# Performance work log

Measured on AMD Instinct MI355X. Metric: run time of the kernel, lower is better.

Reference implementation:

```python
import jax, jax.numpy as jnp
import numpy as np

T, S, B, D, H, FFN = 1024, 1024, 4, 1024, 16, 4096
HD = D // H
EPS = 1e-5


def xavier(key, shape, gain=1.0):
    fan_out, fan_in = shape
    a = gain * np.sqrt(6.0 / (fan_in + fan_out))
    return jax.random.uniform(key, shape, jnp.float32, -a, a)


def layer_norm(x, g, b):
    mu = jnp.mean(x, axis=-1, keepdims=True)
    var = jnp.mean(jnp.square(x - mu), axis=-1, keepdims=True)
    return (x - mu) / jnp.sqrt(var + EPS) * g + b


def mha(q, k, v, Wq, bq, Wk, bk, Wv, bv, Wo, bo, key_padding_mask=None, attn_mask=None):
    # q: [t,b,d]; k,v: [s,b,d]; key_padding_mask: [b,s] bool (True = pad)
    t, b, d = q.shape
    s = v.shape[0]
    if key_padding_mask is not None:
        # original zeroes the KEY tensor before projection
        k = k * (~key_padding_mask).T[:, :, None]
    Q = (q @ Wq.T + bq).reshape(t, b, H, HD)
    K = (k @ Wk.T + bk).reshape(s, b, H, HD)
    V = (v @ Wv.T + bv).reshape(s, b, H, HD)
    scores = jnp.einsum('tbhk,sbhk->bhts', Q, K) / jnp.sqrt(jnp.float32(HD))
    if attn_mask is not None:
        scores = scores + attn_mask  # additive [t,s] broadcast over b,h
    p = jax.nn.softmax(scores, axis=-1)
    ctx = jnp.einsum('bhts,sbhk->tbhk', p, V)  # [t,b,h,hd]
    out = ctx.reshape(t, b, d)
    attn_w = jnp.swapaxes(ctx, 0, 2)  # [h,b,t,hd] as in original
    return out @ Wo.T + bo, attn_w


def setup_inputs() -> dict:
    key = jax.random.key(0)
    ks = jax.random.split(key, 16)
    inv2 = 1.0 / np.sqrt(2.0)
    d = {
        'state': jax.random.normal(ks[0], (T, B, D), jnp.float32),
        'encoder_out': jax.random.normal(ks[1], (S, B, D), jnp.float32),
        'self_attn_mask': jnp.triu(jnp.full((T, T), -1e9, jnp.float32), 1),
        'self_attn_padding_mask': jnp.zeros((B, T), bool),
        'encoder_padding_mask': jnp.broadcast_to(jnp.arange(S)[None, :] >= (S - S // 10), (B, S)),
        # self-attention projections
        'sa_Wq': xavier(ks[2], (D, D), inv2), 'sa_bq': jnp.zeros((D,), jnp.float32),
        'sa_Wk': xavier(ks[3], (D, D), inv2), 'sa_bk': jnp.zeros((D,), jnp.float32),
        'sa_Wv': xavier(ks[4], (D, D), inv2), 'sa_bv': jnp.zeros((D,), jnp.float32),
        'sa_Wo': xavier(ks[5], (D, D)), 'sa_bo': jnp.zeros((D,), jnp.float32),
        # encoder-decoder attention projections
        'ea_Wq': xavier(ks[6], (D, D), inv2), 'ea_bq': jnp.zeros((D,), jnp.float32),
        'ea_Wk': xavier(ks[7], (D, D), inv2), 'ea_bk': jnp.zeros((D,), jnp.float32),
        'ea_Wv': xavier(ks[8], (D, D), inv2), 'ea_bv': jnp.zeros((D,), jnp.float32),
        'ea_Wo': xavier(ks[9], (D, D)), 'ea_bo': jnp.zeros((D,), jnp.float32),
        # layernorms
        'ln1_g': jnp.ones((D,), jnp.float32), 'ln1_b': jnp.zeros((D,), jnp.float32),
        'ln2_g': jnp.ones((D,), jnp.float32), 'ln2_b': jnp.zeros((D,), jnp.float32),
        'ln3_g': jnp.ones((D,), jnp.float32), 'ln3_b': jnp.zeros((D,), jnp.float32),
        # FFN
        'fc1_W': xavier(ks[10], (FFN, D)), 'fc1_b': jnp.zeros((FFN,), jnp.float32),
        'fc2_W': xavier(ks[11], (D, FFN)), 'fc2_b': jnp.zeros((D,), jnp.float32),
    }
    return d


def reference(state, encoder_out, self_attn_mask, self_attn_padding_mask, encoder_padding_mask,
              sa_Wq, sa_bq, sa_Wk, sa_bk, sa_Wv, sa_bv, sa_Wo, sa_bo,
              ea_Wq, ea_bq, ea_Wk, ea_bk, ea_Wv, ea_bv, ea_Wo, ea_bo,
              ln1_g, ln1_b, ln2_g, ln2_b, ln3_g, ln3_b,
              fc1_W, fc1_b, fc2_W, fc2_b):
    x = state
    # self-attention block (dropout is identity in eval)
    res = x
    a, _ = mha(x, x, x, sa_Wq, sa_bq, sa_Wk, sa_bk, sa_Wv, sa_bv, sa_Wo, sa_bo,
               key_padding_mask=self_attn_padding_mask, attn_mask=self_attn_mask)
    x = layer_norm(a + res, ln1_g, ln1_b)
    # encoder-decoder attention block
    res = x
    a, attn = mha(x, encoder_out, encoder_out, ea_Wq, ea_bq, ea_Wk, ea_bk, ea_Wv, ea_bv, ea_Wo, ea_bo,
                  key_padding_mask=encoder_padding_mask, attn_mask=None)
    x = layer_norm(a + res, ln2_g, ln2_b)
    # FFN block
    res = x
    h = jax.nn.relu(x @ fc1_W.T + fc1_b)
    x = layer_norm(h @ fc2_W.T + fc2_b + res, ln3_g, ln3_b)
    return (x, attn)
```

## Files before the change

### kernel.cpp

```cpp
#include <hip/hip_runtime.h>
#include <hip/hip_bf16.h>


typedef __attribute__((ext_vector_type(8))) short bf16x8;
typedef __attribute__((ext_vector_type(4))) float f32x4;
typedef __attribute__((ext_vector_type(8))) unsigned short us8;
typedef __attribute__((ext_vector_type(4))) unsigned short us4;

#define AS1 __attribute__((address_space(1)))
#define AS3 __attribute__((address_space(3)))

#define T_LEN 1024
#define S_LEN 1024
#define B_DIM 4
#define D_MOD 1024
#define H_NUM 16
#define FFN_D 4096
#define NTOK  4096

__device__ __forceinline__ float b2f(unsigned short u) {
    return __uint_as_float(((unsigned int)u) << 16);
}
__device__ __forceinline__ unsigned short f2b(float f) {
    unsigned int x = __float_as_uint(f);
    x += 0x7fffu + ((x >> 16) & 1u);
    return (unsigned short)(x >> 16);
}

struct CvtArgs {
    const float* s[12];
    unsigned short* d[12];
};

__global__ __launch_bounds__(256) void cvt_all_kernel(CvtArgs a)
{
    const int cnt[12] = {2048, 2048, 512, 512, 512, 512, 512, 512, 512, 512, 2048, 2048};
    int bid = blockIdx.x;
    int seg = 0;
    while (bid >= cnt[seg]) { bid -= cnt[seg]; ++seg; }
    const size_t off = (size_t)bid * 2048 + threadIdx.x * 8;
    const float* src = a.s[seg] + off;
    unsigned short* dst = a.d[seg] + off;
    const f32x4 v0 = *(const f32x4*)src;
    const f32x4 v1 = *(const f32x4*)(src + 4);
    us8 o;
#pragma unroll
    for (int j = 0; j < 4; ++j) { o[j] = f2b(v0[j]); o[4 + j] = f2b(v1[j]); }
    *(us8*)dst = o;
}

template <int BN>
__global__ __launch_bounds__(512, 1) void gemm8ph_kernel(
    const unsigned short* __restrict__ A,
    const unsigned short* __restrict__ W,
    const float* __restrict__ b0, const float* __restrict__ b1,
    const float* __restrict__ b2, const float* __restrict__ b3,
    const int* __restrict__ rowmask, unsigned int maskbits,
    unsigned short* __restrict__ p0, unsigned short* __restrict__ p1,
    unsigned short* __restrict__ p2, unsigned short* __restrict__ p3,
    int ostride,
    const float* __restrict__ resid, float* __restrict__ outf,
    float* __restrict__ partf,
    int M, int N, int K, int relu, int ksplit)
{
    constexpr int NR  = BN / 64;
    constexpr int BLH = (BN * 64) / 8192;
    constexpr int BBUF = BN * 128;

    __shared__ __align__(16) char ldsb[65536 + 2 * BBUF];

    const int tid  = threadIdx.x;
    const int lane = tid & 63;
    const int wid  = tid >> 6;
    const int wr   = wid >> 2;
    const int wc   = wid & 3;
    const int row0 = blockIdx.x * 256;
    const int col0 = blockIdx.y * BN;
    const int rsel = lane & 15;
    const int kg2  = (lane >> 4) * 16;
    const int kz   = blockIdx.z;
    const int Keff = K / ksplit;
    const int koff = kz * Keff;
    const int NT   = Keff >> 6;

    f32x4 acc[8][NR];
#pragma unroll
    for (int m = 0; m < 8; ++m)
#pragma unroll
        for (int n = 0; n < NR; ++n)
            acc[m][n] = (f32x4){0.f, 0.f, 0.f, 0.f};

    auto stageA = [&](int buf, int half, int t) {
        const int k0 = koff + (t << 6);
#pragma unroll
        for (int i = 0; i < 2; ++i) {
            const unsigned int beta = (unsigned int)(half * 16384 + i * 8192 + tid * 16);
            const unsigned int lam  = beta ^ (((beta >> 7) & 7u) << 4);
            const char* src = (const char*)A +
                ((size_t)(row0 + (int)(lam >> 7)) * K + k0) * 2 + (lam & 127u);
            __builtin_amdgcn_global_load_lds((const AS1 void*)src,
                (AS3 void*)(ldsb + buf * 32768 + beta), 16, 0, 0);
        }
    };
    auto stageB = [&](int buf, int half, int t) {
        const int k0 = koff + (t << 6);
#pragma unroll
        for (int i = 0; i < BLH; ++i) {
            const unsigned int beta = (unsigned int)(half * (BN * 64) + i * 8192 + tid * 16);
            const unsigned int lam  = beta ^ (((beta >> 7) & 7u) << 4);
            const char* src = (const char*)W +
                ((size_t)(col0 + (int)(lam >> 7)) * K + k0) * 2 + (lam & 127u);
            __builtin_amdgcn_global_load_lds((const AS1 void*)src,
                (AS3 void*)(ldsb + 65536 + buf * BBUF + beta), 16, 0, 0);
        }
    };
    auto readA = [&](int buf, int m, int k) -> bf16x8 {
        const int r = wr * 128 + m * 16 + rsel;
        const unsigned int l  = (unsigned int)(r * 128 + k * 64 + kg2);
        const unsigned int ph = l ^ (((unsigned int)(r & 7)) << 4);
        return *(const bf16x8*)(ldsb + buf * 32768 + ph);
    };
    auto readB = [&](int buf, int n, int k) -> bf16x8 {
        const int r = wc * (BN / 4) + n * 16 + rsel;
        const unsigned int l  = (unsigned int)(r * 128 + k * 64 + kg2);
        const unsigned int ph = l ^ (((unsigned int)(r & 7)) << 4);
        return *(const bf16x8*)(ldsb + 65536 + buf * BBUF + ph);
    };

    stageA(0, 0, 0); stageA(0, 1, 0); stageB(0, 0, 0); stageB(0, 1, 0);
    stageA(1, 0, 1); stageA(1, 1, 1);
    asm volatile("s_waitcnt vmcnt(4)" ::: "memory");
    __builtin_amdgcn_s_barrier();

    bf16x8 Afr[8][2], Bfr[NR][2];

    for (int t = 0; t < NT; ++t) {
        const int cur = t & 1;
#pragma unroll
        for (int m = 0; m < 4; ++m) { Afr[m][0] = readA(cur, m, 0); Afr[m][1] = readA(cur, m, 1); }
#pragma unroll
        for (int n = 0; n < NR; ++n) Bfr[n][0] = readB(cur, n, 0);
        if (t + 1 < NT) stageB(cur ^ 1, 0, t + 1);
        __builtin_amdgcn_s_barrier();
        asm volatile("s_waitcnt lgkmcnt(0)" ::: "memory");
        __builtin_amdgcn_sched_barrier(0);
        __builtin_amdgcn_s_setprio(1);
#pragma unroll
        for (int m = 0; m < 4; ++m)
#pragma unroll
            for (int n = 0; n < NR; ++n)
                acc[m][n] = __builtin_amdgcn_mfma_f32_16x16x32_bf16(Afr[m][0], Bfr[n][0], acc[m][n], 0, 0, 0);
        __builtin_amdgcn_s_setprio(0);
        __builtin_amdgcn_s_barrier();
#pragma unroll
        for (int m = 4; m < 8; ++m) { Afr[m][0] = readA(cur, m, 0); Afr[m][1] = readA(cur, m, 1); }
#pragma unroll
        for (int n = 0; n < NR; ++n) Bfr[n][1] = readB(cur, n, 1);
        if (t + 1 < NT) stageB(cur ^ 1, 1, t + 1);
        __builtin_amdgcn_s_barrier();
        asm volatile("s_waitcnt lgkmcnt(0)" ::: "memory");
        __builtin_amdgcn_sched_barrier(0);
        __builtin_amdgcn_s_setprio(1);
#pragma unroll
        for (int m = 4; m < 8; ++m)
#pragma unroll
            for (int n = 0; n < NR; ++n)
                acc[m][n] = __builtin_amdgcn_mfma_f32_16x16x32_bf16(Afr[m][0], Bfr[n][0], acc[m][n], 0, 0, 0);
        __builtin_amdgcn_s_setprio(0);
        __builtin_amdgcn_s_barrier();
        if (t + 2 < NT) stageA(cur, 0, t + 2);
        __builtin_amdgcn_s_barrier();
        __builtin_amdgcn_s_setprio(1);
#pragma unroll
        for (int m = 0; m < 4; ++m)
#pragma unroll
            for (int n = 0; n < NR; ++n)
                acc[m][n] = __builtin_amdgcn_mfma_f32_16x16x32_bf16(Afr[m][1], Bfr[n][1], acc[m][n], 0, 0, 0);
        __builtin_amdgcn_s_setprio(0);
        __builtin_amdgcn_s_barrier();
        if (t + 2 < NT) stageA(cur, 1, t + 2);
        __builtin_amdgcn_s_barrier();
        __builtin_amdgcn_s_setprio(1);
#pragma unroll
        for (int m = 4; m < 8; ++m)
#pragma unroll
            for (int n = 0; n < NR; ++n)
                acc[m][n] = __builtin_amdgcn_mfma_f32_16x16x32_bf16(Afr[m][1], Bfr[n][1], acc[m][n], 0, 0, 0);
        __builtin_amdgcn_s_setprio(0);
        if (t + 2 < NT) { asm volatile("s_waitcnt vmcnt(4)" ::: "memory"); }
        else            { asm volatile("s_waitcnt vmcnt(0)" ::: "memory"); }
        __builtin_amdgcn_s_barrier();
    }

    const int seq  = M >> 2;
    const int c    = col0 >> 10;
    unsigned short* op = c == 0 ? p0 : c == 1 ? p1 : c == 2 ? p2 : p3;
    const float*    bp = c == 0 ? b0 : c == 1 ? b1 : c == 2 ? b2 : b3;
    const bool um = rowmask && ((maskbits >> c) & 1u);
    const int rbas = (lane >> 4) * 4;
    if (partf && kz > 0) {
#pragma unroll
        for (int m = 0; m < 8; ++m)
#pragma unroll
            for (int n = 0; n < NR; ++n)
#pragma unroll
                for (int j = 0; j < 4; ++j) {
                    const int gr = row0 + wr * 128 + m * 16 + rbas + j;
                    const int gc = col0 + wc * (BN / 4) + n * 16 + rsel;
                    partf[(size_t)gr * N + gc] = acc[m][n][j];
                }
    } else {
#pragma unroll
        for (int m = 0; m < 8; ++m)
#pragma unroll
            for (int n = 0; n < NR; ++n)
#pragma unroll
                for (int j = 0; j < 4; ++j) {
                    const int gr = row0 + wr * 128 + m * 16 + rbas + j;
                    const int gc = col0 + wc * (BN / 4) + n * 16 + rsel;
                    float v = acc[m][n][j];
                    if (um && rowmask[(gr & 3) * seq + (gr >> 2)] != 0) v = 0.f;
                    v += bp[gc & 1023];
                    if (relu) v = fmaxf(v, 0.f);
                    if (resid) v += resid[(size_t)gr * N + gc];
                    if (outf) outf[(size_t)gr * N + gc] = v;
                    else      op[(size_t)gr * ostride + (gc & 1023)] = f2b(v);
                }
    }
}

__global__ __launch_bounds__(256) void vtrans_kernel(
    const unsigned short* __restrict__ Vb, unsigned short* __restrict__ Vt)
{
    __shared__ unsigned short tile[64 * 72];
    const int tid = threadIdx.x;
    const int t0  = blockIdx.x * 64;
    const int bh  = blockIdx.y;
    const int h   = bh & (H_NUM - 1);
    const int b   = bh >> 4;

    const int r   = tid >> 2;
    const int c16 = (tid & 3) * 16;
    const unsigned short* src = Vb + ((size_t)(t0 + r) * B_DIM + b) * D_MOD + h * 64 + c16;
    *(us8*)&tile[r * 72 + c16]     = *(const us8*)src;
    *(us8*)&tile[r * 72 + c16 + 8] = *(const us8*)(src + 8);
    __syncthreads();

    const int dr  = tid >> 2;
    const int tch = (tid & 3) * 16;
    us8 o0, o1;
#pragma unroll
    for (int j = 0; j < 8; ++j) {
        o0[j] = tile[(tch + j) * 72 + dr];
        o1[j] = tile[(tch + 8 + j) * 72 + dr];
    }
    unsigned short* dst = Vt + (size_t)(bh * 64 + dr) * S_LEN + t0 + tch;
    *(us8*)dst       = o0;
    *(us8*)(dst + 8) = o1;
}

__global__ __launch_bounds__(256) void flash_mfma_kernel(
    const unsigned short* __restrict__ Qb,
    const unsigned short* __restrict__ Kb,
    const unsigned short* __restrict__ Vt,
    unsigned short* __restrict__ outc,
    float* __restrict__ outp,
    int causal)
{
    __shared__ __align__(16) unsigned short Ks[32 * 64];
    __shared__ __align__(16) unsigned short Vts[64 * 32];
    __shared__ __align__(16) unsigned short Ps[4 * 16 * 40];

    const int tid  = threadIdx.x;
    const int lane = tid & 63;
    const int wv   = tid >> 6;
    const int g    = lane >> 4;
    const int n    = lane & 15;
    const int t0   = blockIdx.x * 64;
    const int bh   = blockIdx.y;
    const int h    = bh & (H_NUM - 1);
    const int b    = bh >> 4;
    const int woff = wv * 16;

    bf16x8 qa[2];
    {
        const unsigned short* qptr =
            Qb + ((size_t)(t0 + woff + n) * B_DIM + b) * D_MOD + h * 64 + g * 8;
        qa[0] = *(const bf16x8*)qptr;
        qa[1] = *(const bf16x8*)(qptr + 32);
    }

    f32x4 ctx[4];
#pragma unroll
    for (int nt = 0; nt < 4; ++nt) ctx[nt] = (f32x4){0.f, 0.f, 0.f, 0.f};
    float m_run[4], l_run[4];
#pragma unroll
    for (int j = 0; j < 4; ++j) { m_run[j] = -INFINITY; l_run[j] = 0.f; }

    unsigned short* pw = &Ps[wv * 640];
    const int smax = causal ? (t0 + 64) : S_LEN;

    for (int s0 = 0; s0 < smax; s0 += 32) {
        {
            const unsigned int beta = tid * 16;
            const unsigned int lamK = beta ^ (((beta >> 7) & 7u) << 4);
            const unsigned int krow = lamK >> 7, kcolb = lamK & 127u;
            const char* srcK = (const char*)Kb +
                ((size_t)((s0 + krow) * B_DIM + b) * D_MOD + h * 64) * 2 + kcolb;
            __builtin_amdgcn_global_load_lds((const AS1 void*)srcK,
                (AS3 void*)((char*)Ks + beta), 16, 0, 0);
            const unsigned int lamV = beta ^ (((beta >> 6) & 3u) << 4);
            const unsigned int drow = lamV >> 6, scolb = lamV & 63u;
            const char* srcV = (const char*)Vt +
                ((size_t)(bh * 64 + drow) * S_LEN + s0) * 2 + scolb;
            __builtin_amdgcn_global_load_lds((const AS1 void*)srcV,
                (AS3 void*)((char*)Vts + beta), 16, 0, 0);
        }
        __syncthreads();

        f32x4 sacc[2];
        sacc[0] = (f32x4){0.f, 0.f, 0.f, 0.f};
        sacc[1] = (f32x4){0.f, 0.f, 0.f, 0.f};
#pragma unroll
        for (int u = 0; u < 2; ++u) {
#pragma unroll
            for (int kc = 0; kc < 2; ++kc) {
                const unsigned int l = (unsigned int)(u * 16 + n) * 128 + kc * 64 + g * 16;
                const unsigned int ph = l ^ ((unsigned int)(n & 7) << 4);
                const bf16x8 kb = *(const bf16x8*)((const char*)Ks + ph);
                sacc[u] = __builtin_amdgcn_mfma_f32_16x16x32_bf16(qa[kc], kb, sacc[u], 0, 0, 0);
            }
        }

        float e0[4], e1[4], scj[4];
#pragma unroll
        for (int j = 0; j < 4; ++j) {
            float p0 = sacc[0][j] * 0.125f;
            float p1 = sacc[1][j] * 0.125f;
            if (causal) {
                const int tq = t0 + woff + g * 4 + j;
                if (s0 + n > tq)      p0 += -1e9f;
                if (s0 + 16 + n > tq) p1 += -1e9f;
            }
            float mx = fmaxf(p0, p1);
            mx = fmaxf(mx, __shfl_xor(mx, 1));
            mx = fmaxf(mx, __shfl_xor(mx, 2));
            mx = fmaxf(mx, __shfl_xor(mx, 4));
            mx = fmaxf(mx, __shfl_xor(mx, 8));
            const float m_new = fmaxf(m_run[j], mx);
            const float sc = __expf(m_run[j] - m_new);
            m_run[j] = m_new;
            e0[j] = __expf(p0 - m_new);
            e1[j] = __expf(p1 - m_new);
            float ls = e0[j] + e1[j];
            ls += __shfl_xor(ls, 1);
            ls += __shfl_xor(ls, 2);
            ls += __shfl_xor(ls, 4);
            ls += __shfl_xor(ls, 8);
            l_run[j] = l_run[j] * sc + ls;
            scj[j] = sc;
        }
#pragma unroll
        for (int nt = 0; nt < 4; ++nt)
#pragma unroll
            for (int j = 0; j < 4; ++j) ctx[nt][j] *= scj[j];

#pragma unroll
        for (int j = 0; j < 4; ++j) {
            pw[(g * 4 + j) * 40 + n]      = f2b(e0[j]);
            pw[(g * 4 + j) * 40 + 16 + n] = f2b(e1[j]);
        }
        const bf16x8 pa = *(const bf16x8*)&pw[n * 40 + g * 8];

#pragma unroll
        for (int nt = 0; nt < 4; ++nt) {
            const unsigned int l = (unsigned int)(nt * 16 + n) * 64 + g * 16;
            const unsigned int ph = l ^ ((unsigned int)(n & 3) << 4);
            const bf16x8 vb = *(const bf16x8*)((const char*)Vts + ph);
            ctx[nt] = __builtin_amdgcn_mfma_f32_16x16x32_bf16(pa, vb, ctx[nt], 0, 0, 0);
        }
        __syncthreads();
    }

    float inv[4];
#pragma unroll
    for (int j = 0; j < 4; ++j) inv[j] = 1.f / l_run[j];
#pragma unroll
    for (int nt = 0; nt < 4; ++nt) {
#pragma unroll
        for (int j = 0; j < 4; ++j) {
            const int t = t0 + woff + g * 4 + j;
            const int d = nt * 16 + n;
            const float v = ctx[nt][j] * inv[j];
            outc[((size_t)t * B_DIM + b) * D_MOD + h * 64 + d] = f2b(v);
            if (outp)
                outp[((size_t)(h * B_DIM + b) * T_LEN + t) * 64 + d] = v;
        }
    }
}

__global__ __launch_bounds__(256) void layernorm_kernel(
    const float* __restrict__ y,
    const float* __restrict__ part,
    const float* __restrict__ g,
    const float* __restrict__ be,
    float* __restrict__ out_f,
    unsigned short* __restrict__ out_bf)
{
    __shared__ float red[8];
    const int row = blockIdx.x;
    const int tid = threadIdx.x;
    f32x4 v = *(const f32x4*)&y[(size_t)row * D_MOD + tid * 4];
    if (part) {
        const f32x4 pv = *(const f32x4*)&part[(size_t)row * D_MOD + tid * 4];
#pragma unroll
        for (int j = 0; j < 4; ++j) v[j] += pv[j];
    }
    float s = v[0] + v[1] + v[2] + v[3];
#pragma unroll
    for (int o = 32; o > 0; o >>= 1) s += __shfl_xor(s, o);
    if ((tid & 63) == 0) red[tid >> 6] = s;
    __syncthreads();
    const float mu = (red[0] + red[1] + red[2] + red[3]) * (1.f / D_MOD);
    const float d0 = v[0] - mu, d1 = v[1] - mu, d2 = v[2] - mu, d3 = v[3] - mu;
    float s2 = d0 * d0 + d1 * d1 + d2 * d2 + d3 * d3;
#pragma unroll
    for (int o = 32; o > 0; o >>= 1) s2 += __shfl_xor(s2, o);
    if ((tid & 63) == 0) red[4 + (tid >> 6)] = s2;
    __syncthreads();
    const float var  = (red[4] + red[5] + red[6] + red[7]) * (1.f / D_MOD);
    const float rstd = rsqrtf(var + 1e-5f);
    const float dd[4] = {d0, d1, d2, d3};
    f32x4 of;
    us4 ob;
#pragma unroll
    for (int j = 0; j < 4; ++j) {
        const int col = tid * 4 + j;
        const float r = dd[j] * rstd * g[col] + be[col];
        of[j] = r;
        ob[j] = f2b(r);
    }
    const size_t oi = (size_t)row * D_MOD + tid * 4;
    if (out_f)  *(f32x4*)&out_f[oi] = of;
    if (out_bf) *(us4*)&out_bf[oi]  = ob;
}

extern "C" void kernel_launch(void* const* d_in, const int* in_sizes, int n_in,
                              void* d_out, int out_size, void* d_ws, size_t ws_size,
                              hipStream_t stream) {
    (void)in_sizes; (void)n_in; (void)out_size; (void)ws_size;

    const float* x0    = (const float*)d_in[0];
    const float* enc   = (const float*)d_in[1];
    const int* sa_pad  = (const int*)d_in[3];
    const int* ea_pad  = (const int*)d_in[4];
    const float* sa_Wq = (const float*)d_in[5];
    const float* sa_bq = (const float*)d_in[6];
    const float* sa_Wk = (const float*)d_in[7];
    const float* sa_bk = (const float*)d_in[8];
    const float* sa_Wv = (const float*)d_in[9];
    const float* sa_bv = (const float*)d_in[10];
    const float* sa_Wo = (const float*)d_in[11];
    const float* sa_bo = (const float*)d_in[12];
    const float* ea_Wq = (const float*)d_in[13];
    const float* ea_bq = (const float*)d_in[14];
    const float* ea_Wk = (const float*)d_in[15];
    const float* ea_bk = (const float*)d_in[16];
    const float* ea_Wv = (const float*)d_in[17];
    const float* ea_bv = (const float*)d_in[18];
    const float* ea_Wo = (const float*)d_in[19];
    const float* ea_bo = (const float*)d_in[20];
    const float* ln1_g = (const float*)d_in[21];
    const float* ln1_b = (const float*)d_in[22];
    const float* ln2_g = (const float*)d_in[23];
    const float* ln2_b = (const float*)d_in[24];
    const float* ln3_g = (const float*)d_in[25];
    const float* ln3_b = (const float*)d_in[26];
    const float* fc1_W = (const float*)d_in[27];
    const float* fc1_b = (const float*)d_in[28];
    const float* fc2_W = (const float*)d_in[29];
    const float* fc2_b = (const float*)d_in[30];

    const size_t DD = (size_t)D_MOD * D_MOD;
    const size_t FD = (size_t)FFN_D * D_MOD;
    const size_t SL = (size_t)NTOK * D_MOD;

    unsigned short* ws_us = (unsigned short*)d_ws;
    unsigned short* wb[10];
    for (int i = 0; i < 8; ++i) wb[i] = ws_us + i * DD;
    wb[8] = ws_us + 8 * DD;
    wb[9] = ws_us + 8 * DD + FD;
    unsigned short* abf = ws_us + 8 * DD + 2 * FD;
    unsigned short* ebf = abf + SL;
    unsigned short* Cb  = ebf + SL;
    unsigned short* Qb  = Cb + SL;
    unsigned short* Kb  = Qb + SL;
    unsigned short* Vb  = Kb + SL;
    unsigned short* Vt  = Vb + SL;
    unsigned short* Hbf = Qb;
    float* fbase = (float*)(Vt + SL);
    float* Yf  = fbase;
    float* X1f = fbase + SL;
    float* Pq  = (float*)Qb;
    float* Pa  = (float*)abf;

    float* outx = (float*)d_out;
    float* outa = outx + SL;

    const dim3 blk(256);
    const dim3 blk512(512);
    const dim3 g_attn(T_LEN / 64, B_DIM * H_NUM);
    unsigned short* nbf = nullptr;
    float* nff = nullptr;
    const float* nf = nullptr;
    const int* ni = nullptr;

    {
        CvtArgs ca;
        const float* srcs[12]  = {x0, enc, sa_Wq, sa_Wk, sa_Wv, sa_Wo,
                                  ea_Wq, ea_Wk, ea_Wv, ea_Wo, fc1_W, fc2_W};
        unsigned short* dsts[12] = {abf, ebf, wb[0], wb[1], wb[2], wb[3],
                                    wb[4], wb[5], wb[6], wb[7], wb[8], wb[9]};
        for (int i = 0; i < 12; ++i) { ca.s[i] = srcs[i]; ca.d[i] = dsts[i]; }
        cvt_all_kernel<<<dim3(12288), blk, 0, stream>>>(ca);
    }

    gemm8ph_kernel<256><<<dim3(16, 12, 1), blk512, 0, stream>>>(
        abf, wb[0], sa_bq, sa_bk, sa_bv, sa_bv, sa_pad, 0x2u,
        Qb, Kb, Vb, Vb, D_MOD, nf, nff, nff, NTOK, 3072, D_MOD, 0, 1);
    vtrans_kernel<<<g_attn, blk, 0, stream>>>(Vb, Vt);
    flash_mfma_kernel<<<g_attn, blk, 0, stream>>>(Qb, Kb, Vt, Cb, nff, 1);
    gemm8ph_kernel<128><<<dim3(16, 8, 2), blk512, 0, stream>>>(
        Cb, wb[3], sa_bo, sa_bo, sa_bo, sa_bo, ni, 0u,
        nbf, nbf, nbf, nbf, D_MOD, x0, Yf, Pq, NTOK, D_MOD, D_MOD, 0, 2);
    layernorm_kernel<<<dim3(NTOK), blk, 0, stream>>>(Yf, Pq, ln1_g, ln1_b, X1f, abf);

    gemm8ph_kernel<128><<<dim3(16, 8, 1), blk512, 0, stream>>>(
        abf, wb[4], ea_bq, ea_bq, ea_bq, ea_bq, ni, 0u,
        Qb, Qb, Qb, Qb, D_MOD, nf, nff, nff, NTOK, D_MOD, D_MOD, 0, 1);
    gemm8ph_kernel<128><<<dim3(16, 16, 1), blk512, 0, stream>>>(
        ebf, wb[5], ea_bk, ea_bv, ea_bv, ea_bv, ea_pad, 0x1u,
        Kb, Vb, Vb, Vb, D_MOD, nf, nff, nff, NTOK, 2048, D_MOD, 0, 1);
    vtrans_kernel<<<g_attn, blk, 0, stream>>>(Vb, Vt);
    flash_mfma_kernel<<<g_attn, blk, 0, stream>>>(Qb, Kb, Vt, Cb, outa, 0);
    gemm8ph_kernel<128><<<dim3(16, 8, 2), blk512, 0, stream>>>(
        Cb, wb[7], ea_bo, ea_bo, ea_bo, ea_bo, ni, 0u,
        nbf, nbf, nbf, nbf, D_MOD, X1f, Yf, Pq, NTOK, D_MOD, D_MOD, 0, 2);
    layernorm_kernel<<<dim3(NTOK), blk, 0, stream>>>(Yf, Pq, ln2_g, ln2_b, X1f, ebf);

    gemm8ph_kernel<256><<<dim3(16, 16, 1), blk512, 0, stream>>>(
        ebf, wb[8], fc1_b, fc1_b + 1024, fc1_b + 2048, fc1_b + 3072, ni, 0u,
        Hbf, Hbf + 1024, Hbf + 2048, Hbf + 3072, FFN_D, nf, nff, nff,
        NTOK, FFN_D, D_MOD, 1, 1);
    gemm8ph_kernel<128><<<dim3(16, 8, 2), blk512, 0, stream>>>(
        Hbf, wb[9], fc2_b, fc2_b, fc2_b, fc2_b, ni, 0u,
        nbf, nbf, nbf, nbf, D_MOD, X1f, Yf, Pa, NTOK, D_MOD, FFN_D, 0, 2);
    layernorm_kernel<<<dim3(NTOK), blk, 0, stream>>>(Yf, Pa, ln3_g, ln3_b, outx, nbf);
}
```

Before: 703.3 us.

## Double-buffer K/V tiles and widen flash attention key tile to 64

```diff
diff --git a/kernel.cpp b/kernel.cpp
--- a/kernel.cpp
+++ b/kernel.cpp
@@ -259,7 +259,7 @@
     *(us8*)(dst + 8) = o1;
 }
 
-__global__ __launch_bounds__(256) void flash_mfma_kernel(
+__global__ __launch_bounds__(256, 3) void flash_mfma_kernel(
     const unsigned short* __restrict__ Qb,
     const unsigned short* __restrict__ Kb,
     const unsigned short* __restrict__ Vt,
@@ -267,9 +267,9 @@
     float* __restrict__ outp,
     int causal)
 {
-    __shared__ __align__(16) unsigned short Ks[32 * 64];
-    __shared__ __align__(16) unsigned short Vts[64 * 32];
-    __shared__ __align__(16) unsigned short Ps[4 * 16 * 40];
+    __shared__ __align__(16) unsigned short Ks[2][64 * 64];
+    __shared__ __align__(16) unsigned short Vts[2][64 * 64];
+    __shared__ __align__(16) unsigned short Ps[4][16 * 72];
 
     const int tid  = threadIdx.x;
     const int lane = tid & 63;
@@ -297,89 +297,106 @@
 #pragma unroll
     for (int j = 0; j < 4; ++j) { m_run[j] = -INFINITY; l_run[j] = 0.f; }
 
-    unsigned short* pw = &Ps[wv * 640];
+    unsigned short* pw = &Ps[wv][0];
     const int smax = causal ? (t0 + 64) : S_LEN;
-
-    for (int s0 = 0; s0 < smax; s0 += 32) {
-        {
-            const unsigned int beta = tid * 16;
-            const unsigned int lamK = beta ^ (((beta >> 7) & 7u) << 4);
-            const unsigned int krow = lamK >> 7, kcolb = lamK & 127u;
+    const int NTt  = smax >> 6;
+
+    auto stage = [&](int buf, int s0) {
+#pragma unroll
+        for (int i = 0; i < 2; ++i) {
+            const unsigned int beta = (unsigned int)(i * 4096 + tid * 16);
+            const unsigned int lam  = beta ^ (((beta >> 7) & 7u) << 4);
+            const int row = (int)(lam >> 7);
+            const unsigned int colb = lam & 127u;
             const char* srcK = (const char*)Kb +
-                ((size_t)((s0 + krow) * B_DIM + b) * D_MOD + h * 64) * 2 + kcolb;
+                ((size_t)((s0 + row) * B_DIM + b) * D_MOD + h * 64) * 2 + colb;
             __builtin_amdgcn_global_load_lds((const AS1 void*)srcK,
-                (AS3 void*)((char*)Ks + beta), 16, 0, 0);
-            const unsigned int lamV = beta ^ (((beta >> 6) & 3u) << 4);
-            const unsigned int drow = lamV >> 6, scolb = lamV & 63u;
+                (AS3 void*)((char*)&Ks[buf][0] + beta), 16, 0, 0);
             const char* srcV = (const char*)Vt +
-                ((size_t)(bh * 64 + drow) * S_LEN + s0) * 2 + scolb;
+                ((size_t)(bh * 64 + row) * S_LEN + s0) * 2 + colb;
             __builtin_amdgcn_global_load_lds((const AS1 void*)srcV,
-                (AS3 void*)((char*)Vts + beta), 16, 0, 0);
-        }
-        __syncthreads();
-
-        f32x4 sacc[2];
-        sacc[0] = (f32x4){0.f, 0.f, 0.f, 0.f};
-        sacc[1] = (f32x4){0.f, 0.f, 0.f, 0.f};
-#pragma unroll
-        for (int u = 0; u < 2; ++u) {
+                (AS3 void*)((char*)&Vts[buf][0] + beta), 16, 0, 0);
+        }
+    };
+
+    stage(0, 0);
+    for (int t = 0; t < NTt; ++t) {
+        const int s0  = t << 6;
+        const int cur = t & 1;
+        asm volatile("s_waitcnt vmcnt(0)" ::: "memory");
+        __builtin_amdgcn_s_barrier();
+        if (t + 1 < NTt) stage(cur ^ 1, s0 + 64);
+
+        f32x4 sacc[4];
+#pragma unroll
+        for (int u = 0; u < 4; ++u) sacc[u] = (f32x4){0.f, 0.f, 0.f, 0.f};
+#pragma unroll
+        for (int u = 0; u < 4; ++u) {
 #pragma unroll
             for (int kc = 0; kc < 2; ++kc) {
-                const unsigned int l = (unsigned int)(u * 16 + n) * 128 + kc * 64 + g * 16;
-                const unsigned int ph = l ^ ((unsigned int)(n & 7) << 4);
-                const bf16x8 kb = *(const bf16x8*)((const char*)Ks + ph);
+                const int r = u * 16 + n;
+                const unsigned int l  = (unsigned int)(r * 128 + kc * 64 + g * 16);
+                const unsigned int ph = l ^ (((unsigned int)(r & 7)) << 4);
+                const bf16x8 kb = *(const bf16x8*)((const char*)&Ks[cur][0] + ph);
                 sacc[u] = __builtin_amdgcn_mfma_f32_16x16x32_bf16(qa[kc], kb, sacc[u], 0, 0, 0);
             }
         }
 
-        float e0[4], e1[4], scj[4];
+        const bool diag = causal && (s0 + 64 > t0);
+        float scj[4];
 #pragma unroll
         for (int j = 0; j < 4; ++j) {
-            float p0 = sacc[0][j] * 0.125f;
-            float p1 = sacc[1][j] * 0.125f;
-            if (causal) {
+            float p[4];
+#pragma unroll
+            for (int u = 0; u < 4; ++u) p[u] = sacc[u][j] * 0.125f;
+            if (diag) {
                 const int tq = t0 + woff + g * 4 + j;
-                if (s0 + n > tq)      p0 += -1e9f;
-                if (s0 + 16 + n > tq) p1 += -1e9f;
+#pragma unroll
+                for (int u = 0; u < 4; ++u)
+                    if (s0 + u * 16 + n > tq) p[u] += -1e9f;
             }
-            float mx = fmaxf(p0, p1);
-            mx = fmaxf(mx, __shfl_xor(mx, 1));
-            mx = fmaxf(mx, __shfl_xor(mx, 2));
-            mx = fmaxf(mx, __shfl_xor(mx, 4));
-            mx = fmaxf(mx, __shfl_xor(mx, 8));
-            const float m_new = fmaxf(m_run[j], mx);
+            float pm = fmaxf(fmaxf(p[0], p[1]), fmaxf(p[2], p[3]));
+            pm = fmaxf(pm, __shfl_xor(pm, 1));
+            pm = fmaxf(pm, __shfl_xor(pm, 2));
+            pm = fmaxf(pm, __shfl_xor(pm, 4));
+            pm = fmaxf(pm, __shfl_xor(pm, 8));
+            const float m_new = fmaxf(m_run[j], pm);
             const float sc = __expf(m_run[j] - m_new);
             m_run[j] = m_new;
-            e0[j] = __expf(p0 - m_new);
-            e1[j] = __expf(p1 - m_new);
-            float ls = e0[j] + e1[j];
+            float e[4];
+#pragma unroll
+            for (int u = 0; u < 4; ++u) e[u] = __expf(p[u] - m_new);
+            float ls = (e[0] + e[1]) + (e[2] + e[3]);
             ls += __shfl_xor(ls, 1);
             ls += __shfl_xor(ls, 2);
             ls += __shfl_xor(ls, 4);
             ls += __shfl_xor(ls, 8);
             l_run[j] = l_run[j] * sc + ls;
             scj[j] = sc;
+#pragma unroll
+            for (int u = 0; u < 4; ++u)
+                pw[(g * 4 + j) * 72 + u * 16 + n] = f2b(e[u]);
         }
 #pragma unroll
         for (int nt = 0; nt < 4; ++nt)
 #pragma unroll
             for (int j = 0; j < 4; ++j) ctx[nt][j] *= scj[j];
 
-#pragma unroll
-        for (int j = 0; j < 4; ++j) {
-            pw[(g * 4 + j) * 40 + n]      = f2b(e0[j]);
-            pw[(g * 4 + j) * 40 + 16 + n] = f2b(e1[j]);
-        }
-        const bf16x8 pa = *(const bf16x8*)&pw[n * 40 + g * 8];
-
+        bf16x8 pa[2];
+#pragma unroll
+        for (int ks = 0; ks < 2; ++ks)
+            pa[ks] = *(const bf16x8*)&pw[n * 72 + ks * 32 + g * 8];
 #pragma unroll
         for (int nt = 0; nt < 4; ++nt) {
-            const unsigned int l = (unsigned int)(nt * 16 + n) * 64 + g * 16;
-            const unsigned int ph = l ^ ((unsigned int)(n & 3) << 4);
-            const bf16x8 vb = *(const bf16x8*)((const char*)Vts + ph);
-            ctx[nt] = __builtin_amdgcn_mfma_f32_16x16x32_bf16(pa, vb, ctx[nt], 0, 0, 0);
-        }
-        __syncthreads();
+#pragma unroll
+            for (int ks = 0; ks < 2; ++ks) {
+                const int r = nt * 16 + n;
+                const unsigned int l  = (unsigned int)(r * 128 + ks * 64 + g * 16);
+                const unsigned int ph = l ^ (((unsigned int)(r & 7)) << 4);
+                const bf16x8 vb = *(const bf16x8*)((const char*)&Vts[cur][0] + ph);
+                ctx[nt] = __builtin_amdgcn_mfma_f32_16x16x32_bf16(pa[ks], vb, ctx[nt], 0, 0, 0);
+            }
+        }
     }
 
     float inv[4];
```

Measured after the change: 683.6 us. 1.03x faster.
